# Optimization experiments

Hardware: AMD Instinct MI355X
Metric: run time of the kernel (lower is better)

Reference implementation:

```python
import jax, jax.numpy as jnp
import numpy as np

BATCH, SEQ, H, N = 8, 4096, 512, 64
DT_MIN, DT_MAX = 1e-3, 1e-1


def setup_inputs() -> dict:
    key = jax.random.key(0)
    k1, k2, k3, k4, k5 = jax.random.split(key, 5)
    n = jnp.arange(N, dtype=jnp.float32)
    # HiPPO-LegS diagonal: A[n,n] = -(n+1) -> log|diag(A)| = log(n+1)
    A_log = jnp.broadcast_to(jnp.log(n + 1.0), (H, N))
    Bv = jnp.broadcast_to(jnp.sqrt(2.0 * n + 1.0), (H, N))
    C = jax.random.normal(k1, (H, N), dtype=jnp.float32) * 0.01
    D = jnp.ones((H,), dtype=jnp.float32)
    log_dt = jax.random.uniform(k2, (H,), dtype=jnp.float32) * (
        np.log(DT_MAX) - np.log(DT_MIN)) + np.log(DT_MIN)
    # reverse-direction params (bidirectional)
    A_log_r = A_log
    B_r = Bv
    C_r = jax.random.normal(k3, (H, N), dtype=jnp.float32) * 0.01
    # out_bi Linear: weight [H, 2H], bias [H]
    W_bi = jax.random.normal(k4, (H, 2 * H), dtype=jnp.float32) / np.sqrt(2.0 * H)
    b_bi = jnp.zeros((H,), dtype=jnp.float32)
    u = jax.random.normal(k5, (BATCH, SEQ, H), dtype=jnp.float32)
    return {"u": u, "A_log": A_log, "Bv": Bv, "C": C, "D": D,
            "log_dt": log_dt, "A_log_r": A_log_r, "B_r": B_r, "C_r": C_r,
            "W_bi": W_bi, "b_bi": b_bi}


def _conv(u, A_log, Bp, Cp, D, log_dt):
    """Diagonal SSM as FFT convolution. u: [B, L, H]."""
    L = u.shape[1]
    dt = jnp.exp(log_dt)                      # [H]
    eA = jnp.exp(A_log)                       # [H, N]
    A_bar = jnp.exp(-dt[:, None] * eA)        # [H, N]
    B_bar = (A_bar - 1.0) / (-eA) * Bp        # [H, N]
    # log-space power kernel: A_bar^k = exp(k * log A_bar)
    logA = jnp.log(jnp.clip(A_bar, 1e-30, None))
    ks = jnp.arange(L, dtype=u.dtype)
    pows = jnp.exp(ks[None, None, :] * logA[:, :, None])   # [H, N, L]
    K = jnp.einsum('dn,dnl->dl', Cp * B_bar, pows)          # [H, L]
    n_fft = 2 * L
    u_f = jnp.fft.rfft(u, n=n_fft, axis=1)                  # [B, L+1, H] complex
    K_f = jnp.fft.rfft(K, n=n_fft, axis=-1)                 # [H, L+1]
    y = jnp.fft.irfft(u_f * K_f.T[None], n=n_fft, axis=1)[:, :L, :]
    return y + u * D


def reference(u, A_log, Bv, C, D, log_dt, A_log_r, B_r, C_r, W_bi, b_bi):
    y = _conv(u, A_log, Bv, C, D, log_dt)
    yr = jnp.flip(_conv(jnp.flip(u, 1), A_log_r, B_r, C_r, D, log_dt), 1)
    ycat = jnp.concatenate([y, yr], axis=-1)                # [B, L, 2H]
    return ycat @ W_bi.T + b_bi
```

## Files before the change

kernel.cpp:

```cpp
#include <hip/hip_runtime.h>
#include <hip/hip_bf16.h>
#include <stdint.h>

#define L_SEQ  4096
#define H_DIM  512
#define N_ST   64
#define N_B    8
#define N_CH   16
#define T_CH   256
#define K_GEMM 1024

typedef float  f32x4  __attribute__((ext_vector_type(4)));
typedef __bf16 bf16x8 __attribute__((ext_vector_type(8)));
typedef __bf16 bf16x4 __attribute__((ext_vector_type(4)));
typedef unsigned short u16x8 __attribute__((ext_vector_type(8)));
typedef unsigned long long ull;

#define GLOAD16(g, l) __builtin_amdgcn_global_load_lds( \
    (const __attribute__((address_space(1))) void*)(g), \
    (__attribute__((address_space(3))) void*)(l), 16, 0, 0)

__global__ __launch_bounds__(256) void k_ut(
    const float* __restrict__ u, __bf16* __restrict__ ut,
    const float* __restrict__ W, __bf16* __restrict__ Wbf,
    const float* __restrict__ A_log, const float* __restrict__ Bv,
    const float* __restrict__ C, const float* __restrict__ log_dt,
    const float* __restrict__ A_log_r, const float* __restrict__ B_r,
    const float* __restrict__ C_r,
    float* __restrict__ kk, float* __restrict__ pLG,
    float* __restrict__ pCB, float* __restrict__ pPW)
{
    __shared__ float tl[32][65];
    __shared__ float scb[64], slg[64];
    int blk = blockIdx.x;
    int t = threadIdx.x;

    if (blk >= 8192) {
        int dirh = blk - 8192;
        int dir  = dirh >> 9, h = dirh & 511;
        int d = t;
        if (d < 64) {
            int n = d;
            float dt = expf(log_dt[h]);
            const float* Al = dir ? A_log_r : A_log;
            const float* Bp = dir ? B_r    : Bv;
            const float* Cp = dir ? C_r    : C;
            float eA = expf(Al[h * N_ST + n]);
            float Ab = expf(-dt * eA);
            float Bb = (1.0f - Ab) / eA * Bp[h * N_ST + n];
            float cb = Cp[h * N_ST + n] * Bb;
            float lg = -dt * eA * 1.44269504088896f;
            scb[n] = cb; slg[n] = lg;
            pCB[dirh * 64 + n] = cb;
            pLG[dirh * 64 + n] = lg;
            pPW[dirh * 64 + n] = expf(-dt * eA * (float)T_CH);
        }
        __syncthreads();
        float s = 0.f;
        #pragma unroll
        for (int n = 0; n < 64; ++n) s += scb[n] * exp2f((float)d * slg[n]);
        kk[dirh * 256 + d] = s;
        return;
    }

    int lt = blk & 127, ht = (blk >> 7) & 7, b = blk >> 10;
    int ho = t & 63, li = t >> 6;
    #pragma unroll
    for (int it = 0; it < 8; ++it) {
        int l = it * 4 + li;
        tl[l][ho] = u[(size_t)(b * L_SEQ + lt * 32 + l) * H_DIM + ht * 64 + ho];
    }
    if (blk < 2048) {
        int i = blk * 256 + t;
        Wbf[i] = (__bf16)W[i];
    }
    __syncthreads();
    int hh = t >> 2, lrun = (t & 3) * 8;
    bf16x8 v;
    #pragma unroll
    for (int i = 0; i < 8; ++i) v[i] = (__bf16)tl[lrun + i][hh];
    *(bf16x8*)(ut + (size_t)(ht * 64 + hh) * 32768 + b * 4096 + lt * 32 + lrun) = v;
}

__global__ __launch_bounds__(512, 2) void k_state(
    const __bf16* __restrict__ ut, const float* __restrict__ pLG,
    const float* __restrict__ pPW, __bf16* __restrict__ S2)
{
    __shared__ __bf16 uts[16384];
    int h = blockIdx.x;
    int t = threadIdx.x;
    int lane = t & 63, w = t >> 6;
    int lr = lane & 15, lg = lane >> 4;
    int dir = w >> 2, mtile = w & 3;

    float s = pLG[(size_t)(dir * 512 + h) * 64 + mtile * 16 + lr];
    f32x4 pw4 = *(const f32x4*)(pPW + (size_t)(dir * 512 + h) * 64 + mtile * 16 + lg * 4);

    bf16x8 Mf[8];
    #pragma unroll
    for (int kk = 0; kk < 8; ++kk) {
        #pragma unroll
        for (int jj = 0; jj < 8; ++jj) {
            int j = kk * 32 + lg * 8 + jj;
            float e = dir ? (float)j : (float)(255 - j);
            Mf[kk][jj] = (__bf16)exp2f(e * s);
        }
    }

    for (int hf = 0; hf < 2; ++hf) {
        if (hf) __syncthreads();
        #pragma unroll
        for (int i = 0; i < 4; ++i) {
            int chunk = i * 512 + t;
            int col   = chunk >> 5;
            int l8    = (chunk & 31) << 3;
            int l8s   = l8 ^ ((col & 7) << 3);
            GLOAD16(ut + (size_t)h * 32768 + (hf * 64 + col) * 256 + l8s,
                    (char*)uts + chunk * 16);
        }
        __syncthreads();

        #pragma unroll
        for (int ntile = 0; ntile < 4; ++ntile) {
            f32x4 acc = {};
            #pragma unroll
            for (int kk = 0; kk < 8; ++kk) {
                int col = ntile * 16 + lr;
                bf16x8 bv = *(const bf16x8*)((char*)uts + col * 512
                             + (((kk * 4 + lg) ^ (col & 7)) << 4));
                acc = __builtin_amdgcn_mfma_f32_16x16x32_bf16(Mf[kk], bv, acc, 0, 0, 0);
            }
            f32x4 X;
            if (dir == 0) {
                f32x4 incl = acc;
                float p0 = pw4[0], p1 = pw4[1], p2 = pw4[2], p3 = pw4[3];
                #pragma unroll
                for (int st = 1; st <= 8; st <<= 1) {
                    float u0 = __shfl(incl[0], (lane - st) & 63);
                    float u1 = __shfl(incl[1], (lane - st) & 63);
                    float u2 = __shfl(incl[2], (lane - st) & 63);
                    float u3 = __shfl(incl[3], (lane - st) & 63);
                    if (lr >= st) {
                        incl[0] = fmaf(p0, u0, incl[0]);
                        incl[1] = fmaf(p1, u1, incl[1]);
                        incl[2] = fmaf(p2, u2, incl[2]);
                        incl[3] = fmaf(p3, u3, incl[3]);
                    }
                    p0 *= p0; p1 *= p1; p2 *= p2; p3 *= p3;
                }
                #pragma unroll
                for (int r = 0; r < 4; ++r) {
                    float sh = __shfl(incl[r], (lane - 1) & 63);
                    X[r] = (lr == 0) ? 0.f : sh;
                }
            } else {
                f32x4 incl = acc;
                float p0 = pw4[0], p1 = pw4[1], p2 = pw4[2], p3 = pw4[3];
                #pragma unroll
                for (int st = 1; st <= 8; st <<= 1) {
                    float u0 = __shfl(incl[0], (lane + st) & 63);
                    float u1 = __shfl(incl[1], (lane + st) & 63);
                    float u2 = __shfl(incl[2], (lane + st) & 63);
                    float u3 = __shfl(incl[3], (lane + st) & 63);
                    if (lr <= 15 - st) {
                        incl[0] = fmaf(p0, u0, incl[0]);
                        incl[1] = fmaf(p1, u1, incl[1]);
                        incl[2] = fmaf(p2, u2, incl[2]);
                        incl[3] = fmaf(p3, u3, incl[3]);
                    }
                    p0 *= p0; p1 *= p1; p2 *= p2; p3 *= p3;
                }
                #pragma unroll
                for (int r = 0; r < 4; ++r) {
                    float sh = __shfl(incl[r], (lane + 1) & 63);
                    X[r] = (lr == 15) ? 0.f : sh;
                }
            }
            int colg = hf * 64 + ntile * 16 + lr;
            int nq   = mtile * 4 + lg;
            bf16x4 o;
            #pragma unroll
            for (int r = 0; r < 4; ++r) o[r] = (__bf16)X[r];
            *(bf16x4*)(S2 + ((size_t)((dir * 512 + h) * 16 + nq) * 128 + colg) * 4) = o;
        }
    }
}

template<int DIR>
__device__ __forceinline__ void conv_body(
    int h, int t,
    const float* __restrict__ kk, const float* __restrict__ pLG,
    const float* __restrict__ pCB, const float* __restrict__ Dv,
    const __bf16* __restrict__ ut, const __bf16* __restrict__ S,
    __bf16* __restrict__ ycT,
    __bf16* uts, ull* kkq8, unsigned short* asc, float* slg, float* scb)
{
    int dirh = DIR * 512 + h;
    int lane = t & 63, w = t >> 6;
    int lr = lane & 15, lg = lane >> 4;

    #pragma unroll
    for (int hf = 0; hf < 2; ++hf)
        #pragma unroll
        for (int i = 0; i < 4; ++i) {
            int chunk = i * 512 + t;
            int col   = chunk >> 5;
            int l8    = (chunk & 31) << 3;
            int l8s   = l8 ^ ((col & 7) << 3);
            GLOAD16(ut + (size_t)h * 32768 + (hf * 64 + col) * 256 + l8s,
                    (char*)uts + hf * 32768 + chunk * 16);
        }

    for (int i = t; i < 548; i += 512) {
        int d = DIR ? (i - 272) : (271 - i);
        float kv = (d >= 0 && d < 256) ? kk[dirh * 256 + d] : 0.f;
        asc[i] = __builtin_bit_cast(unsigned short, (__bf16)kv);
    }
    if (t < 64)       slg[t]      = pLG[dirh * 64 + t];
    else if (t < 128) scb[t - 64] = pCB[dirh * 64 + (t - 64)];
    asm volatile("s_waitcnt lgkmcnt(0)" ::: "memory");
    __builtin_amdgcn_sched_barrier(0);
    __builtin_amdgcn_s_barrier();
    __builtin_amdgcn_sched_barrier(0);
    for (int i = t; i < 544; i += 512)
        kkq8[i] = (ull)asc[i] | ((ull)asc[i+1] << 16) | ((ull)asc[i+2] << 32)
                | ((ull)asc[i+3] << 48);

    bf16x8 gvv[2][2];
    #pragma unroll
    for (int nt = 0; nt < 2; ++nt)
        #pragma unroll
        for (int mf = 0; mf < 2; ++mf) {
            int rt = mf ? (15 - w) : w;
            int l  = rt * 16 + lr;
            float e = DIR ? (float)(256 - l) : (float)(l + 1);
            #pragma unroll
            for (int j = 0; j < 8; ++j) {
                int n = nt * 32 + lg * 8 + j;
                gvv[nt][mf][j] = (__bf16)(scb[n] * exp2f(e * slg[n]));
            }
        }

    float Dh = Dv[h];
    const ull* kq = kkq8;

    asm volatile("s_waitcnt vmcnt(4) lgkmcnt(0)" ::: "memory");
    __builtin_amdgcn_sched_barrier(0);
    __builtin_amdgcn_s_barrier();
    __builtin_amdgcn_sched_barrier(0);

    const int rt0 = w, rt1 = 15 - w;
    const int sb0 = (DIR ? 272 : 271) + lg * 8 - rt0 * 16 - lr;
    const int sb1 = (DIR ? 272 : 271) + lg * 8 - rt1 * 16 - lr;
    const int jhi0 = DIR ? 8 : ((rt0 >> 1) + 1);
    const int jlo1 = DIR ? (rt1 >> 1) : 0;
    const int jbeg = DIR ? (rt0 >> 1) : 0;
    const int jend = DIR ? 8 : (((rt1) >> 1) + 1);

    #pragma unroll
    for (int hf = 0; hf < 2; ++hf) {
        if (hf) __syncthreads();
        char* ub = (char*)uts + hf * 32768;

        f32x4 acc[2][4] = {};

        for (int jt = jbeg; jt < jend; ++jt) {
            bf16x8 bv[4];
            #pragma unroll
            for (int n = 0; n < 4; ++n) {
                int col = n * 16 + lr;
                bv[n] = *(const bf16x8*)(ub + col * 512
                          + (((jt * 4 + lg) ^ (col & 7)) << 4));
            }
            if (DIR ? true : (jt < jhi0)) {
                int si = sb0 + jt * 32;
                ull lo = kq[si], hi = kq[si + 4];
                bf16x8 av;
                ((ull*)&av)[0] = lo; ((ull*)&av)[1] = hi;
                __builtin_amdgcn_s_setprio(1);
                #pragma unroll
                for (int n = 0; n < 4; ++n)
                    acc[0][n] = __builtin_amdgcn_mfma_f32_16x16x32_bf16(av, bv[n], acc[0][n], 0, 0, 0);
                __builtin_amdgcn_s_setprio(0);
            }
            if (DIR ? (jt >= jlo1) : true) {
                int si = sb1 + jt * 32;
                ull lo = kq[si], hi = kq[si + 4];
                bf16x8 av;
                ((ull*)&av)[0] = lo; ((ull*)&av)[1] = hi;
                __builtin_amdgcn_s_setprio(1);
                #pragma unroll
                for (int n = 0; n < 4; ++n)
                    acc[1][n] = __builtin_amdgcn_mfma_f32_16x16x32_bf16(av, bv[n], acc[1][n], 0, 0, 0);
                __builtin_amdgcn_s_setprio(0);
            }
        }

        #pragma unroll
        for (int nt = 0; nt < 2; ++nt) {
            bf16x8 bs[4];
            #pragma unroll
            for (int n = 0; n < 4; ++n) {
                int colg = (hf * 4 + n) * 16 + lr;
                int nq0  = nt * 8 + lg * 2;
                const __bf16* sp = S + ((size_t)((DIR * 512 + h) * 16 + nq0) * 128 + colg) * 4;
                bf16x4 s0 = *(const bf16x4*)(sp);
                bf16x4 s1 = *(const bf16x4*)(sp + 512);
                #pragma unroll
                for (int j = 0; j < 4; ++j) { bs[n][j] = s0[j]; bs[n][4 + j] = s1[j]; }
            }
            __builtin_amdgcn_s_setprio(1);
            #pragma unroll
            for (int mf = 0; mf < 2; ++mf)
                #pragma unroll
                for (int n = 0; n < 4; ++n)
                    acc[mf][n] = __builtin_amdgcn_mfma_f32_16x16x32_bf16(gvv[nt][mf], bs[n], acc[mf][n], 0, 0, 0);
            __builtin_amdgcn_s_setprio(0);
        }

        #pragma unroll
        for (int mf = 0; mf < 2; ++mf) {
            int rt = mf ? rt1 : rt0;
            int l0 = rt * 16 + lg * 4;
            #pragma unroll
            for (int n = 0; n < 4; ++n) {
                int col = n * 16 + lr;
                bf16x4 uv = *(const bf16x4*)(ub + col * 512
                             + ((((l0 >> 3) ^ (col & 7)) << 4) | ((l0 & 7) * 2)));
                bf16x4 o;
                #pragma unroll
                for (int r = 0; r < 4; ++r)
                    o[r] = (__bf16)(acc[mf][n][r] + Dh * (float)uv[r]);
                *(bf16x4*)(ycT + (size_t)dirh * 32768 + (hf * 64 + col) * 256 + l0) = o;
            }
        }
    }
}

__global__ __launch_bounds__(512, 4) void k_conv(
    const float* __restrict__ kk, const float* __restrict__ pLG,
    const float* __restrict__ pCB, const float* __restrict__ Dv,
    const __bf16* __restrict__ ut, const __bf16* __restrict__ S,
    __bf16* __restrict__ ycT)
{
    __shared__ __bf16 uts[32768];
    __shared__ ull kkq8[544];
    __shared__ unsigned short asc[548];
    __shared__ float slg[64], scb[64];
    int h = blockIdx.x & 511;
    int t = threadIdx.x;
    if (blockIdx.x >> 9)
        conv_body<1>(h, t, kk, pLG, pCB, Dv, ut, S, ycT, uts, kkq8, asc, slg, scb);
    else
        conv_body<0>(h, t, kk, pLG, pCB, Dv, ut, S, ycT, uts, kkq8, asc, slg, scb);
}

__global__ __launch_bounds__(256, 2) void k_gemm(
    const __bf16* __restrict__ ycT, const __bf16* __restrict__ B,
    const float* __restrict__ bias, float* __restrict__ out)
{
    __shared__ __bf16 As[2][4][128][8];
    __shared__ __bf16 Bs[4][256][32];
    int t  = threadIdx.x;
    int l  = t & 63, w = t >> 6;
    int lr = l & 15, lg = l >> 4;
    int bid   = blockIdx.y * 2 + blockIdx.x;
    int swzid = (bid & 7) * 64 + (bid >> 3);
    int mBase = (swzid >> 1) * 128;
    int nBase = (swzid & 1) * 256;
    int wr = (w >> 1) * 64, wc = (w & 1) * 128;

    int sT  = t & 15;
    int sp  = t >> 4;
    int swz  = (sT & 7) << 4;
    int kgrp = sp >> 2;
    int keb  = (sp & 3) * 4;

    f32x4 acc[4][8] = {};
    const __bf16* aptr = ycT + mBase + sT * 8;

#define STAGE_A(abuf, va0, va1) do { \
    char* AsB_ = (char*)&As[0][0][0][0] + (abuf) * 8192; \
    _Pragma("unroll") \
    for (int i = 0; i < 8; ++i) { \
        unsigned v_ = (unsigned)(unsigned short)(va0)[i] \
                    | ((unsigned)(unsigned short)(va1)[i] << 16); \
        int off_ = ((kgrp * 128 + sT * 8 + i) * 16 + keb) ^ swz; \
        *(unsigned*)(AsB_ + off_) = v_; \
    } } while (0)

#define STAGE_B(bbuf, kt_) do { \
    char* BsB_ = (char*)&Bs[0][0][0] + (bbuf) * 16384; \
    _Pragma("unroll") \
    for (int i = 0; i < 4; ++i) { \
        int chunk_ = i * 256 + t; \
        int row_ = chunk_ >> 2, kq_ = chunk_ & 3; \
        int kqs_ = kq_ ^ ((row_ >> 1) & 3); \
        GLOAD16(B + (size_t)(nBase + row_) * K_GEMM + (kt_) + kqs_ * 8, \
                BsB_ + chunk_ * 16); \
    } } while (0)

#define COMPUTE(abuf, bbuf) do { \
    char* AsB_ = (char*)&As[0][0][0][0] + (abuf) * 8192; \
    char* BsB_ = (char*)&Bs[0][0][0] + (bbuf) * 16384; \
    bf16x8 af_[4], bfv_[8]; \
    _Pragma("unroll") \
    for (int m = 0; m < 4; ++m) { \
        int row_ = wr + m * 16 + lr; \
        int off_ = ((lg * 128 + row_) * 16) ^ (((row_ >> 3) & 7) << 4); \
        af_[m] = *(const bf16x8*)(AsB_ + off_); \
    } \
    _Pragma("unroll") \
    for (int n = 0; n < 8; ++n) { \
        int row_ = wc + n * 16 + lr; \
        bfv_[n] = *(const bf16x8*)(BsB_ + row_ * 64 \
                    + ((lg * 16) ^ (((row_ >> 1) & 3) << 4))); \
    } \
    __builtin_amdgcn_s_setprio(1); \
    _Pragma("unroll") \
    for (int m = 0; m < 4; ++m) \
        _Pragma("unroll") \
        for (int n = 0; n < 8; ++n) \
            acc[m][n] = __builtin_amdgcn_mfma_f32_16x16x32_bf16(af_[m], bfv_[n], acc[m][n], 0, 0, 0); \
    __builtin_amdgcn_s_setprio(0); \
    } while (0)

    u16x8 a0 = *(const u16x8*)(aptr + (size_t)(2 * sp) * 32768);
    u16x8 a1 = *(const u16x8*)(aptr + (size_t)(2 * sp + 1) * 32768);
    STAGE_B(0, 0);
    STAGE_B(1, 32);

    int ab = 0;
    for (int i = 0; i < 30; ++i) {
        int kt = i * 32;
        STAGE_A(ab, a0, a1);
        a0 = *(const u16x8*)(aptr + (size_t)(kt + 32 + 2 * sp) * 32768);
        a1 = *(const u16x8*)(aptr + (size_t)(kt + 32 + 2 * sp + 1) * 32768);
        STAGE_B((i + 2) & 3, kt + 64);
        asm volatile("s_waitcnt vmcnt(10) lgkmcnt(0)" ::: "memory");
        __builtin_amdgcn_sched_barrier(0);
        __builtin_amdgcn_s_barrier();
        __builtin_amdgcn_sched_barrier(0);
        COMPUTE(ab, i & 3);
        ab ^= 1;
    }
    STAGE_A(ab, a0, a1);
    a0 = *(const u16x8*)(aptr + (size_t)(992 + 2 * sp) * 32768);
    a1 = *(const u16x8*)(aptr + (size_t)(992 + 2 * sp + 1) * 32768);
    asm volatile("s_waitcnt vmcnt(6) lgkmcnt(0)" ::: "memory");
    __builtin_amdgcn_sched_barrier(0);
    __builtin_amdgcn_s_barrier();
    __builtin_amdgcn_sched_barrier(0);
    COMPUTE(ab, 30 & 3);
    ab ^= 1;
    STAGE_A(ab, a0, a1);
    asm volatile("s_waitcnt vmcnt(0) lgkmcnt(0)" ::: "memory");
    __builtin_amdgcn_sched_barrier(0);
    __builtin_amdgcn_s_barrier();
    __builtin_amdgcn_sched_barrier(0);
    COMPUTE(ab, 31 & 3);

#undef STAGE_A
#undef STAGE_B
#undef COMPUTE

    #pragma unroll
    for (int n = 0; n < 8; ++n) {
        int colg = nBase + wc + n * 16 + lr;
        float bv = bias[colg];
        #pragma unroll
        for (int m = 0; m < 4; ++m) {
            int rowg = mBase + wr + m * 16 + lg * 4;
            #pragma unroll
            for (int r = 0; r < 4; ++r)
                out[(size_t)(rowg + r) * H_DIM + colg] = acc[m][n][r] + bv;
        }
    }
}

extern "C" void kernel_launch(void* const* d_in, const int* in_sizes, int n_in,
                              void* d_out, int out_size, void* d_ws, size_t ws_size,
                              hipStream_t stream)
{
    const float* u       = (const float*)d_in[0];
    const float* A_log   = (const float*)d_in[1];
    const float* Bv      = (const float*)d_in[2];
    const float* C       = (const float*)d_in[3];
    const float* D       = (const float*)d_in[4];
    const float* log_dt  = (const float*)d_in[5];
    const float* A_log_r = (const float*)d_in[6];
    const float* B_r     = (const float*)d_in[7];
    const float* C_r     = (const float*)d_in[8];
    const float* W_bi    = (const float*)d_in[9];
    const float* b_bi    = (const float*)d_in[10];
    float* out = (float*)d_out;

    char* ws = (char*)d_ws;
    float* pCB  = (float*)(ws + 0x040000);
    float* pPW  = (float*)(ws + 0x080000);
    float* pLG  = (float*)(ws + 0x0C0000);
    float* kk   = (float*)(ws + 0x100000);
    __bf16* Wbf = (__bf16*)(ws + 0x200000);
    __bf16* S   = (__bf16*)(ws + 0x300000);
    __bf16* ut  = (__bf16*)(ws + 0x1300000);
    __bf16* ycT = (__bf16*)(ws + 0x3300000);

    k_ut   <<<9216, 256, 0, stream>>>(u, ut, W_bi, Wbf,
                                      A_log, Bv, C, log_dt, A_log_r, B_r, C_r,
                                      kk, pLG, pCB, pPW);
    k_state<<<512,  512, 0, stream>>>(ut, pLG, pPW, S);
    k_conv <<<1024, 512, 0, stream>>>(kk, pLG, pCB, D, ut, S, ycT);
    dim3 g(2, 256);
    k_gemm <<<g,    256, 0, stream>>>(ycT, Wbf, b_bi, out);
}
```

Before: 126.3 us.

## Fuse forward and reverse conv directions into one block sharing the LDS input tile

```diff
diff --git a/kernel.cpp b/kernel.cpp
--- a/kernel.cpp
+++ b/kernel.cpp
@@ -186,158 +186,7 @@
     }
 }
 
-template<int DIR>
-__device__ __forceinline__ void conv_body(
-    int h, int t,
-    const float* __restrict__ kk, const float* __restrict__ pLG,
-    const float* __restrict__ pCB, const float* __restrict__ Dv,
-    const __bf16* __restrict__ ut, const __bf16* __restrict__ S,
-    __bf16* __restrict__ ycT,
-    __bf16* uts, ull* kkq8, unsigned short* asc, float* slg, float* scb)
-{
-    int dirh = DIR * 512 + h;
-    int lane = t & 63, w = t >> 6;
-    int lr = lane & 15, lg = lane >> 4;
-
-    #pragma unroll
-    for (int hf = 0; hf < 2; ++hf)
-        #pragma unroll
-        for (int i = 0; i < 4; ++i) {
-            int chunk = i * 512 + t;
-            int col   = chunk >> 5;
-            int l8    = (chunk & 31) << 3;
-            int l8s   = l8 ^ ((col & 7) << 3);
-            GLOAD16(ut + (size_t)h * 32768 + (hf * 64 + col) * 256 + l8s,
-                    (char*)uts + hf * 32768 + chunk * 16);
-        }
-
-    for (int i = t; i < 548; i += 512) {
-        int d = DIR ? (i - 272) : (271 - i);
-        float kv = (d >= 0 && d < 256) ? kk[dirh * 256 + d] : 0.f;
-        asc[i] = __builtin_bit_cast(unsigned short, (__bf16)kv);
-    }
-    if (t < 64)       slg[t]      = pLG[dirh * 64 + t];
-    else if (t < 128) scb[t - 64] = pCB[dirh * 64 + (t - 64)];
-    asm volatile("s_waitcnt lgkmcnt(0)" ::: "memory");
-    __builtin_amdgcn_sched_barrier(0);
-    __builtin_amdgcn_s_barrier();
-    __builtin_amdgcn_sched_barrier(0);
-    for (int i = t; i < 544; i += 512)
-        kkq8[i] = (ull)asc[i] | ((ull)asc[i+1] << 16) | ((ull)asc[i+2] << 32)
-                | ((ull)asc[i+3] << 48);
-
-    bf16x8 gvv[2][2];
-    #pragma unroll
-    for (int nt = 0; nt < 2; ++nt)
-        #pragma unroll
-        for (int mf = 0; mf < 2; ++mf) {
-            int rt = mf ? (15 - w) : w;
-            int l  = rt * 16 + lr;
-            float e = DIR ? (float)(256 - l) : (float)(l + 1);
-            #pragma unroll
-            for (int j = 0; j < 8; ++j) {
-                int n = nt * 32 + lg * 8 + j;
-                gvv[nt][mf][j] = (__bf16)(scb[n] * exp2f(e * slg[n]));
-            }
-        }
-
-    float Dh = Dv[h];
-    const ull* kq = kkq8;
-
-    asm volatile("s_waitcnt vmcnt(4) lgkmcnt(0)" ::: "memory");
-    __builtin_amdgcn_sched_barrier(0);
-    __builtin_amdgcn_s_barrier();
-    __builtin_amdgcn_sched_barrier(0);
-
-    const int rt0 = w, rt1 = 15 - w;
-    const int sb0 = (DIR ? 272 : 271) + lg * 8 - rt0 * 16 - lr;
-    const int sb1 = (DIR ? 272 : 271) + lg * 8 - rt1 * 16 - lr;
-    const int jhi0 = DIR ? 8 : ((rt0 >> 1) + 1);
-    const int jlo1 = DIR ? (rt1 >> 1) : 0;
-    const int jbeg = DIR ? (rt0 >> 1) : 0;
-    const int jend = DIR ? 8 : (((rt1) >> 1) + 1);
-
-    #pragma unroll
-    for (int hf = 0; hf < 2; ++hf) {
-        if (hf) __syncthreads();
-        char* ub = (char*)uts + hf * 32768;
-
-        f32x4 acc[2][4] = {};
-
-        for (int jt = jbeg; jt < jend; ++jt) {
-            bf16x8 bv[4];
-            #pragma unroll
-            for (int n = 0; n < 4; ++n) {
-                int col = n * 16 + lr;
-                bv[n] = *(const bf16x8*)(ub + col * 512
-                          + (((jt * 4 + lg) ^ (col & 7)) << 4));
-            }
-            if (DIR ? true : (jt < jhi0)) {
-                int si = sb0 + jt * 32;
-                ull lo = kq[si], hi = kq[si + 4];
-                bf16x8 av;
-                ((ull*)&av)[0] = lo; ((ull*)&av)[1] = hi;
-                __builtin_amdgcn_s_setprio(1);
-                #pragma unroll
-                for (int n = 0; n < 4; ++n)
-                    acc[0][n] = __builtin_amdgcn_mfma_f32_16x16x32_bf16(av, bv[n], acc[0][n], 0, 0, 0);
-                __builtin_amdgcn_s_setprio(0);
-            }
-            if (DIR ? (jt >= jlo1) : true) {
-                int si = sb1 + jt * 32;
-                ull lo = kq[si], hi = kq[si + 4];
-                bf16x8 av;
-                ((ull*)&av)[0] = lo; ((ull*)&av)[1] = hi;
-                __builtin_amdgcn_s_setprio(1);
-                #pragma unroll
-                for (int n = 0; n < 4; ++n)
-                    acc[1][n] = __builtin_amdgcn_mfma_f32_16x16x32_bf16(av, bv[n], acc[1][n], 0, 0, 0);
-                __builtin_amdgcn_s_setprio(0);
-            }
-        }
-
-        #pragma unroll
-        for (int nt = 0; nt < 2; ++nt) {
-            bf16x8 bs[4];
-            #pragma unroll
-            for (int n = 0; n < 4; ++n) {
-                int colg = (hf * 4 + n) * 16 + lr;
-                int nq0  = nt * 8 + lg * 2;
-                const __bf16* sp = S + ((size_t)((DIR * 512 + h) * 16 + nq0) * 128 + colg) * 4;
-                bf16x4 s0 = *(const bf16x4*)(sp);
-                bf16x4 s1 = *(const bf16x4*)(sp + 512);
-                #pragma unroll
-                for (int j = 0; j < 4; ++j) { bs[n][j] = s0[j]; bs[n][4 + j] = s1[j]; }
-            }
-            __builtin_amdgcn_s_setprio(1);
-            #pragma unroll
-            for (int mf = 0; mf < 2; ++mf)
-                #pragma unroll
-                for (int n = 0; n < 4; ++n)
-                    acc[mf][n] = __builtin_amdgcn_mfma_f32_16x16x32_bf16(gvv[nt][mf], bs[n], acc[mf][n], 0, 0, 0);
-            __builtin_amdgcn_s_setprio(0);
-        }
-
-        #pragma unroll
-        for (int mf = 0; mf < 2; ++mf) {
-            int rt = mf ? rt1 : rt0;
-            int l0 = rt * 16 + lg * 4;
-            #pragma unroll
-            for (int n = 0; n < 4; ++n) {
-                int col = n * 16 + lr;
-                bf16x4 uv = *(const bf16x4*)(ub + col * 512
-                             + ((((l0 >> 3) ^ (col & 7)) << 4) | ((l0 & 7) * 2)));
-                bf16x4 o;
-                #pragma unroll
-                for (int r = 0; r < 4; ++r)
-                    o[r] = (__bf16)(acc[mf][n][r] + Dh * (float)uv[r]);
-                *(bf16x4*)(ycT + (size_t)dirh * 32768 + (hf * 64 + col) * 256 + l0) = o;
-            }
-        }
-    }
-}
-
-__global__ __launch_bounds__(512, 4) void k_conv(
+__global__ __launch_bounds__(512, 2) void k_conv(
     const float* __restrict__ kk, const float* __restrict__ pLG,
     const float* __restrict__ pCB, const float* __restrict__ Dv,
     const __bf16* __restrict__ ut, const __bf16* __restrict__ S,
@@ -347,12 +196,155 @@
     __shared__ ull kkq8[544];
     __shared__ unsigned short asc[548];
     __shared__ float slg[64], scb[64];
-    int h = blockIdx.x & 511;
+    int h = blockIdx.x;
     int t = threadIdx.x;
-    if (blockIdx.x >> 9)
-        conv_body<1>(h, t, kk, pLG, pCB, Dv, ut, S, ycT, uts, kkq8, asc, slg, scb);
-    else
-        conv_body<0>(h, t, kk, pLG, pCB, Dv, ut, S, ycT, uts, kkq8, asc, slg, scb);
+    int lane = t & 63, w = t >> 6;
+    int lr = lane & 15, lg = lane >> 4;
+
+    #pragma unroll
+    for (int hf = 0; hf < 2; ++hf)
+        #pragma unroll
+        for (int i = 0; i < 4; ++i) {
+            int chunk = i * 512 + t;
+            int col   = chunk >> 5;
+            int l8    = (chunk & 31) << 3;
+            int l8s   = l8 ^ ((col & 7) << 3);
+            GLOAD16(ut + (size_t)h * 32768 + (hf * 64 + col) * 256 + l8s,
+                    (char*)uts + hf * 32768 + chunk * 16);
+        }
+
+    float Dh = Dv[h];
+
+    #pragma unroll
+    for (int dir = 0; dir < 2; ++dir) {
+        int dirh = dir * 512 + h;
+
+        for (int i = t; i < 548; i += 512) {
+            int d = dir ? (i - 272) : (271 - i);
+            float kv = (d >= 0 && d < 256) ? kk[dirh * 256 + d] : 0.f;
+            asc[i] = __builtin_bit_cast(unsigned short, (__bf16)kv);
+        }
+        if (t < 64)       slg[t]      = pLG[dirh * 64 + t];
+        else if (t < 128) scb[t - 64] = pCB[dirh * 64 + (t - 64)];
+        asm volatile("s_waitcnt lgkmcnt(0)" ::: "memory");
+        __builtin_amdgcn_sched_barrier(0);
+        __builtin_amdgcn_s_barrier();
+        __builtin_amdgcn_sched_barrier(0);
+        for (int i = t; i < 544; i += 512)
+            kkq8[i] = (ull)asc[i] | ((ull)asc[i+1] << 16) | ((ull)asc[i+2] << 32)
+                    | ((ull)asc[i+3] << 48);
+
+        bf16x8 gvv[2][2];
+        #pragma unroll
+        for (int nt = 0; nt < 2; ++nt)
+            #pragma unroll
+            for (int mf = 0; mf < 2; ++mf) {
+                int rt = mf ? (15 - w) : w;
+                int l  = rt * 16 + lr;
+                float e = dir ? (float)(256 - l) : (float)(l + 1);
+                #pragma unroll
+                for (int j = 0; j < 8; ++j) {
+                    int n = nt * 32 + lg * 8 + j;
+                    gvv[nt][mf][j] = (__bf16)(scb[n] * exp2f(e * slg[n]));
+                }
+            }
+
+        if (dir == 0) {
+            asm volatile("s_waitcnt vmcnt(0) lgkmcnt(0)" ::: "memory");
+        } else {
+            asm volatile("s_waitcnt lgkmcnt(0)" ::: "memory");
+        }
+        __builtin_amdgcn_sched_barrier(0);
+        __builtin_amdgcn_s_barrier();
+        __builtin_amdgcn_sched_barrier(0);
+
+        const ull* kq = kkq8;
+        const int rt0 = w, rt1 = 15 - w;
+        const int sb0 = (dir ? 272 : 271) + lg * 8 - rt0 * 16 - lr;
+        const int sb1 = (dir ? 272 : 271) + lg * 8 - rt1 * 16 - lr;
+        const int jhi0 = dir ? 8 : ((rt0 >> 1) + 1);
+        const int jlo1 = dir ? (rt1 >> 1) : 0;
+        const int jbeg = dir ? (rt0 >> 1) : 0;
+        const int jend = dir ? 8 : (((rt1) >> 1) + 1);
+
+        #pragma unroll
+        for (int hf = 0; hf < 2; ++hf) {
+            char* ub = (char*)uts + hf * 32768;
+
+            f32x4 acc[2][4] = {};
+
+            for (int jt = jbeg; jt < jend; ++jt) {
+                bf16x8 bv[4];
+                #pragma unroll
+                for (int n = 0; n < 4; ++n) {
+                    int col = n * 16 + lr;
+                    bv[n] = *(const bf16x8*)(ub + col * 512
+                              + (((jt * 4 + lg) ^ (col & 7)) << 4));
+                }
+                if (dir ? true : (jt < jhi0)) {
+                    int si = sb0 + jt * 32;
+                    ull lo = kq[si], hi = kq[si + 4];
+                    bf16x8 av;
+                    ((ull*)&av)[0] = lo; ((ull*)&av)[1] = hi;
+                    __builtin_amdgcn_s_setprio(1);
+                    #pragma unroll
+                    for (int n = 0; n < 4; ++n)
+                        acc[0][n] = __builtin_amdgcn_mfma_f32_16x16x32_bf16(av, bv[n], acc[0][n], 0, 0, 0);
+                    __builtin_amdgcn_s_setprio(0);
+                }
+                if (dir ? (jt >= jlo1) : true) {
+                    int si = sb1 + jt * 32;
+                    ull lo = kq[si], hi = kq[si + 4];
+                    bf16x8 av;
+                    ((ull*)&av)[0] = lo; ((ull*)&av)[1] = hi;
+                    __builtin_amdgcn_s_setprio(1);
+                    #pragma unroll
+                    for (int n = 0; n < 4; ++n)
+                        acc[1][n] = __builtin_amdgcn_mfma_f32_16x16x32_bf16(av, bv[n], acc[1][n], 0, 0, 0);
+                    __builtin_amdgcn_s_setprio(0);
+                }
+            }
+
+            #pragma unroll
+            for (int nt = 0; nt < 2; ++nt) {
+                bf16x8 bs[4];
+                #pragma unroll
+                for (int n = 0; n < 4; ++n) {
+                    int colg = (hf * 4 + n) * 16 + lr;
+                    int nq0  = nt * 8 + lg * 2;
+                    const __bf16* sp = S + ((size_t)((dir * 512 + h) * 16 + nq0) * 128 + colg) * 4;
+                    bf16x4 s0 = *(const bf16x4*)(sp);
+                    bf16x4 s1 = *(const bf16x4*)(sp + 512);
+                    #pragma unroll
+                    for (int j = 0; j < 4; ++j) { bs[n][j] = s0[j]; bs[n][4 + j] = s1[j]; }
+                }
+                __builtin_amdgcn_s_setprio(1);
+                #pragma unroll
+                for (int mf = 0; mf < 2; ++mf)
+                    #pragma unroll
+                    for (int n = 0; n < 4; ++n)
+                        acc[mf][n] = __builtin_amdgcn_mfma_f32_16x16x32_bf16(gvv[nt][mf], bs[n], acc[mf][n], 0, 0, 0);
+                __builtin_amdgcn_s_setprio(0);
+            }
+
+            #pragma unroll
+            for (int mf = 0; mf < 2; ++mf) {
+                int rt = mf ? rt1 : rt0;
+                int l0 = rt * 16 + lg * 4;
+                #pragma unroll
+                for (int n = 0; n < 4; ++n) {
+                    int col = n * 16 + lr;
+                    bf16x4 uv = *(const bf16x4*)(ub + col * 512
+                                 + ((((l0 >> 3) ^ (col & 7)) << 4) | ((l0 & 7) * 2)));
+                    bf16x4 o;
+                    #pragma unroll
+                    for (int r = 0; r < 4; ++r)
+                        o[r] = (__bf16)(acc[mf][n][r] + Dh * (float)uv[r]);
+                    *(bf16x4*)(ycT + (size_t)dirh * 32768 + (hf * 64 + col) * 256 + l0) = o;
+                }
+            }
+        }
+    }
 }
 
 __global__ __launch_bounds__(256, 2) void k_gemm(
@@ -509,7 +501,7 @@
                                       A_log, Bv, C, log_dt, A_log_r, B_r, C_r,
                                       kk, pLG, pCB, pPW);
     k_state<<<512,  512, 0, stream>>>(ut, pLG, pPW, S);
-    k_conv <<<1024, 512, 0, stream>>>(kk, pLG, pCB, D, ut, S, ycT);
+    k_conv <<<512,  512, 0, stream>>>(kk, pLG, pCB, D, ut, S, ycT);
     dim3 g(2, 256);
     k_gemm <<<g,    256, 0, stream>>>(ycT, Wbf, b_bi, out);
 }
```

New measurement: 123.9 us, median of 3. No clear change (-1.9%).
